# Performance work log

Measured on AMD Instinct MI355X. Metric: run time of the kernel, lower is better.

## Reference

```python
import jax, jax.numpy as jnp
import numpy as np

D_MODEL = 768
NHEAD = 12
HEAD_DIM = D_MODEL // NHEAD


def setup_inputs() -> dict:
    key = jax.random.key(0)
    ks = jax.random.split(key, 7)
    s = 1.0 / np.sqrt(D_MODEL)
    x = jax.random.normal(ks[0], (8, 1024, D_MODEL), dtype=jnp.float32)
    Wq = jax.random.uniform(ks[1], (D_MODEL, D_MODEL), jnp.float32, -s, s)
    bq = jax.random.uniform(ks[2], (D_MODEL,), jnp.float32, -s, s)
    Wk = jax.random.uniform(ks[3], (D_MODEL, D_MODEL), jnp.float32, -s, s)
    bk = jax.random.uniform(ks[4], (D_MODEL,), jnp.float32, -s, s)
    Wv = jax.random.uniform(ks[5], (D_MODEL, D_MODEL), jnp.float32, -s, s)
    bv = jax.random.uniform(ks[6], (D_MODEL,), jnp.float32, -s, s)
    return {"x": x, "Wq": Wq, "bq": bq, "Wk": Wk, "bk": bk, "Wv": Wv, "bv": bv}


def reference(x, Wq, bq, Wk, bk, Wv, bv):
    B, S, D = x.shape
    # linear projections (torch Linear: x @ W.T + b)
    q = x @ Wq.T + bq
    k = x @ Wk.T + bk
    v = x @ Wv.T + bv
    # split heads: [B, S, H, Dh] -> [B, H, S, Dh]
    split = lambda t: t.reshape(B, S, NHEAD, HEAD_DIM).transpose(0, 2, 1, 3)
    q, k, v = split(q), split(k), split(v)
    scale = 1.0 / np.sqrt(HEAD_DIM)
    scores = jnp.einsum("bhqd,bhkd->bhqk", q, k) * scale  # [B,H,S,S]
    scores = jax.nn.softmax(scores, axis=-1)  # dropout p=0.0 -> identity
    h = jnp.einsum("bhqk,bhkd->bhqd", scores, v)  # [B,H,S,Dh]
    h = h.transpose(0, 2, 1, 3).reshape(B, S, D)
    return (h, scores)
```

## Files before the change

kernel.cpp:

```cpp
#include <hip/hip_runtime.h>

#define D_MODEL  768
#define NHEAD    12
#define HEAD_DIM 64
#define SEQ      1024
#define BATCH    8
#define NTOK     8192

typedef unsigned short u16;
typedef unsigned int   u32;
typedef float  f32x4  __attribute__((ext_vector_type(4)));
typedef __bf16 bf16x8 __attribute__((ext_vector_type(8)));

#define MFMA(a, b, c) __builtin_amdgcn_mfma_f32_16x16x32_bf16((a), (b), (c), 0, 0, 0)

__device__ __forceinline__ u16 f2bf(float f) {
    u32 u = __float_as_uint(f);
    u += 0x7fffu + ((u >> 16) & 1u);
    return (u16)(u >> 16);
}
__device__ __forceinline__ u32 pack2(float a, float b) {
    return (u32)f2bf(a) | ((u32)f2bf(b) << 16);
}
__device__ __forceinline__ bf16x8 ldfrag(const u16* p) {
    union { uint4 u; bf16x8 b; } c;
    c.u = *(const uint4*)p;
    return c.b;
}

__global__ __launch_bounds__(256)
void qkv_gemm(const float* __restrict__ x,
              const float* __restrict__ Wq, const float* __restrict__ bq,
              const float* __restrict__ Wk, const float* __restrict__ bk,
              const float* __restrict__ Wv, const float* __restrict__ bv,
              u16* __restrict__ qo, u16* __restrict__ ko, u16* __restrict__ vto)
{
    const int m0 = blockIdx.x * 64;
    const int n0 = blockIdx.y * 64;
    const int z  = blockIdx.z;
    const float* W    = (z == 0) ? Wq : (z == 1) ? Wk : Wv;
    const float* bias = (z == 0) ? bq : (z == 1) ? bk : bv;

    __shared__ u16 As[64][72];
    __shared__ u16 Bs[64][72];

    const int t    = threadIdx.x;
    const int lane = t & 63, wave = t >> 6;
    const int grp  = lane >> 4, l16 = lane & 15;
    const int wm   = (wave >> 1) * 32;
    const int wn   = (wave & 1) * 32;
    const int sr   = t >> 2;
    const int sc   = (t & 3) * 16;

    f32x4 acc[2][2] = {};

    for (int kt = 0; kt < D_MODEL; kt += 64) {
        const float* xp = x + (size_t)(m0 + sr) * D_MODEL + kt + sc;
        const float* wp = W + (size_t)(n0 + sr) * D_MODEL + kt + sc;
        const float4 x0 = ((const float4*)xp)[0], x1 = ((const float4*)xp)[1];
        const float4 x2 = ((const float4*)xp)[2], x3 = ((const float4*)xp)[3];
        const float4 w0 = ((const float4*)wp)[0], w1 = ((const float4*)wp)[1];
        const float4 w2 = ((const float4*)wp)[2], w3 = ((const float4*)wp)[3];
        __syncthreads();
        uint4 ua, ub;
        ua.x = pack2(x0.x, x0.y); ua.y = pack2(x0.z, x0.w);
        ua.z = pack2(x1.x, x1.y); ua.w = pack2(x1.z, x1.w);
        ub.x = pack2(x2.x, x2.y); ub.y = pack2(x2.z, x2.w);
        ub.z = pack2(x3.x, x3.y); ub.w = pack2(x3.z, x3.w);
        *(uint4*)&As[sr][sc]     = ua;
        *(uint4*)&As[sr][sc + 8] = ub;
        ua.x = pack2(w0.x, w0.y); ua.y = pack2(w0.z, w0.w);
        ua.z = pack2(w1.x, w1.y); ua.w = pack2(w1.z, w1.w);
        ub.x = pack2(w2.x, w2.y); ub.y = pack2(w2.z, w2.w);
        ub.z = pack2(w3.x, w3.y); ub.w = pack2(w3.z, w3.w);
        *(uint4*)&Bs[sr][sc]     = ua;
        *(uint4*)&Bs[sr][sc + 8] = ub;
        __syncthreads();
#pragma unroll
        for (int ks = 0; ks < 64; ks += 32) {
            const bf16x8 a0 = ldfrag(&As[wm + l16][ks + grp * 8]);
            const bf16x8 a1 = ldfrag(&As[wm + 16 + l16][ks + grp * 8]);
            const bf16x8 b0 = ldfrag(&Bs[wn + l16][ks + grp * 8]);
            const bf16x8 b1 = ldfrag(&Bs[wn + 16 + l16][ks + grp * 8]);
            acc[0][0] = MFMA(a0, b0, acc[0][0]);
            acc[0][1] = MFMA(a0, b1, acc[0][1]);
            acc[1][0] = MFMA(a1, b0, acc[1][0]);
            acc[1][1] = MFMA(a1, b1, acc[1][1]);
        }
    }

    u16* qk_out = (z == 0) ? qo : ko;
#pragma unroll
    for (int tn = 0; tn < 2; ++tn) {
        const int col = n0 + wn + tn * 16 + l16;
        const float bcol = bias[col];
#pragma unroll
        for (int tm = 0; tm < 2; ++tm) {
#pragma unroll
            for (int r = 0; r < 4; ++r) {
                const int row = m0 + wm + tm * 16 + grp * 4 + r;
                const u16 hv = f2bf(acc[tm][tn][r] + bcol);
                if (z < 2) {
                    qk_out[(size_t)row * D_MODEL + col] = hv;
                } else {
                    const int hh = col >> 6, dd = col & 63;
                    const int bb = row >> 10, ss = row & 1023;
                    vto[(((size_t)(bb * NHEAD + hh)) * HEAD_DIM + dd) * SEQ + ss] = hv;
                }
            }
        }
    }
}

__global__ __launch_bounds__(256)
void attn_mfma(const u16* __restrict__ qb, const u16* __restrict__ kb,
               const u16* __restrict__ vtb, float* __restrict__ hout,
               float* __restrict__ sout)
{
    const int qt = blockIdx.x, h = blockIdx.y, b = blockIdx.z;
    const int t    = threadIdx.x;
    const int lane = t & 63, wave = t >> 6;
    const int grp  = lane >> 4, l16 = lane & 15;

    __shared__ u16 Qs[64][72];
    __shared__ u16 Ks[64][72];
    __shared__ u16 Vts[64][72];
    __shared__ u16 Ps[4][16][40];

    const size_t tok0 = (size_t)b * SEQ + qt * 64;
    const int    hb   = h * HEAD_DIM;
    const int    lr   = t >> 3, c0 = (t & 7) * 8;

    {
        const u16* qp = qb + (tok0 + lr) * D_MODEL + hb + c0;
        const uint4 v0 = *(const uint4*)qp;
        const uint4 v1 = *(const uint4*)(qp + (size_t)32 * D_MODEL);
        *(uint4*)&Qs[lr][c0]      = v0;
        *(uint4*)&Qs[lr + 32][c0] = v1;
    }
    __syncthreads();
    const bf16x8 qa0 = ldfrag(&Qs[wave * 16 + l16][grp * 8]);
    const bf16x8 qa1 = ldfrag(&Qs[wave * 16 + l16][32 + grp * 8]);

    const float scale = 0.125f;
    float ssum[4] = {0.f, 0.f, 0.f, 0.f};

    for (int kt = 0; kt < 16; ++kt) {
        __syncthreads();
        {
            const u16* kp = kb + ((size_t)b * SEQ + kt * 64 + lr) * D_MODEL + hb + c0;
            const uint4 v0 = *(const uint4*)kp;
            const uint4 v1 = *(const uint4*)(kp + (size_t)32 * D_MODEL);
            *(uint4*)&Ks[lr][c0]      = v0;
            *(uint4*)&Ks[lr + 32][c0] = v1;
        }
        __syncthreads();
#pragma unroll
        for (int ti = 0; ti < 4; ++ti) {
            const bf16x8 kb0 = ldfrag(&Ks[ti * 16 + l16][grp * 8]);
            const bf16x8 kb1 = ldfrag(&Ks[ti * 16 + l16][32 + grp * 8]);
            f32x4 c = {0.f, 0.f, 0.f, 0.f};
            c = MFMA(qa0, kb0, c);
            c = MFMA(qa1, kb1, c);
#pragma unroll
            for (int r = 0; r < 4; ++r) ssum[r] += __expf(c[r] * scale);
        }
    }
#pragma unroll
    for (int off = 1; off < 16; off <<= 1)
#pragma unroll
        for (int r = 0; r < 4; ++r) ssum[r] += __shfl_xor(ssum[r], off);
    float sinv[4];
#pragma unroll
    for (int r = 0; r < 4; ++r) sinv[r] = 1.0f / ssum[r];

    f32x4 accO[4] = {};
    float* sp = sout + (size_t)(b * NHEAD + h) * SEQ * SEQ;

    for (int kt = 0; kt < 16; ++kt) {
        __syncthreads();
        {
            const u16* kp = kb + ((size_t)b * SEQ + kt * 64 + lr) * D_MODEL + hb + c0;
            const uint4 v0 = *(const uint4*)kp;
            const uint4 v1 = *(const uint4*)(kp + (size_t)32 * D_MODEL);
            *(uint4*)&Ks[lr][c0]      = v0;
            *(uint4*)&Ks[lr + 32][c0] = v1;
            const u16* vp = vtb + ((size_t)(b * NHEAD + h) * HEAD_DIM + lr) * SEQ + kt * 64 + c0;
            const uint4 u0 = *(const uint4*)vp;
            const uint4 u1 = *(const uint4*)(vp + (size_t)32 * SEQ);
            *(uint4*)&Vts[lr][c0]      = u0;
            *(uint4*)&Vts[lr + 32][c0] = u1;
        }
        __syncthreads();
#pragma unroll
        for (int half = 0; half < 2; ++half) {
#pragma unroll
            for (int sub = 0; sub < 2; ++sub) {
                const int ti = half * 2 + sub;
                const bf16x8 kb0 = ldfrag(&Ks[ti * 16 + l16][grp * 8]);
                const bf16x8 kb1 = ldfrag(&Ks[ti * 16 + l16][32 + grp * 8]);
                f32x4 c = {0.f, 0.f, 0.f, 0.f};
                c = MFMA(qa0, kb0, c);
                c = MFMA(qa1, kb1, c);
#pragma unroll
                for (int r = 0; r < 4; ++r) {
                    const float p = __expf(c[r] * scale) * sinv[r];
                    const int qrow = qt * 64 + wave * 16 + grp * 4 + r;
                    sp[(size_t)qrow * SEQ + kt * 64 + ti * 16 + l16] = p;
                    Ps[wave][grp * 4 + r][sub * 16 + l16] = f2bf(p);
                }
            }
            const bf16x8 pa = ldfrag(&Ps[wave][l16][grp * 8]);
#pragma unroll
            for (int c4 = 0; c4 < 4; ++c4) {
                const bf16x8 vb = ldfrag(&Vts[c4 * 16 + l16][half * 32 + grp * 8]);
                accO[c4] = MFMA(pa, vb, accO[c4]);
            }
        }
    }

#pragma unroll
    for (int c4 = 0; c4 < 4; ++c4)
#pragma unroll
        for (int r = 0; r < 4; ++r)
            hout[(tok0 + wave * 16 + grp * 4 + r) * D_MODEL + hb + c4 * 16 + l16] =
                accO[c4][r];
}

extern "C" void kernel_launch(void* const* d_in, const int* in_sizes, int n_in,
                              void* d_out, int out_size, void* d_ws, size_t ws_size,
                              hipStream_t stream)
{
    const float* x  = (const float*)d_in[0];
    const float* Wq = (const float*)d_in[1];
    const float* bq = (const float*)d_in[2];
    const float* Wk = (const float*)d_in[3];
    const float* bk = (const float*)d_in[4];
    const float* Wv = (const float*)d_in[5];
    const float* bv = (const float*)d_in[6];

    float* hout = (float*)d_out;
    float* sout = hout + (size_t)NTOK * D_MODEL;

    u16* qbuf  = (u16*)d_ws;
    u16* kbuf  = qbuf + (size_t)NTOK * D_MODEL;
    u16* vtbuf = kbuf + (size_t)NTOK * D_MODEL;

    qkv_gemm<<<dim3(NTOK / 64, D_MODEL / 64, 3), 256, 0, stream>>>(
        x, Wq, bq, Wk, bk, Wv, bv, qbuf, kbuf, vtbuf);
    attn_mfma<<<dim3(SEQ / 64, NHEAD, BATCH), 256, 0, stream>>>(
        qbuf, kbuf, vtbuf, hout, sout);
}
```

Baseline: 646.7 us.

## Fuse softmax passes into one, deferring normalization and buffering probabilities in registers

Removes the separate first pass over K that only computed softmax row sums. Unnormalized exp values are now accumulated into row sums and fed to the PV MFMA in a single sweep, with the 1/sum normalization applied to the output at the end. The bf16 probability fragments are kept in 32 uint4 registers and written to the scores output afterwards as normalized float4 stores. This roughly halves the QK^T MFMA, exp and K-load work, and makes the score stores vectorized. In exchange, register pressure rises a lot under launch_bounds(256,2), so spills are possible, and the scores output is now rounded to bf16 precision instead of being exact fp32.

```diff
diff --git a/kernel.cpp b/kernel.cpp
--- a/kernel.cpp
+++ b/kernel.cpp
@@ -27,6 +27,13 @@
     c.u = *(const uint4*)p;
     return c.b;
 }
+__device__ __forceinline__ bf16x8 u2b(uint4 u) {
+    union { uint4 u; bf16x8 b; } c;
+    c.u = u;
+    return c.b;
+}
+__device__ __forceinline__ float bflo(u32 u) { return __uint_as_float(u << 16); }
+__device__ __forceinline__ float bfhi(u32 u) { return __uint_as_float(u & 0xffff0000u); }
 
 __global__ __launch_bounds__(256)
 void qkv_gemm(const float* __restrict__ x,
@@ -112,7 +119,7 @@
     }
 }
 
-__global__ __launch_bounds__(256)
+__global__ __launch_bounds__(256, 2)
 void attn_mfma(const u16* __restrict__ qb, const u16* __restrict__ kb,
                const u16* __restrict__ vtb, float* __restrict__ hout,
                float* __restrict__ sout)
@@ -144,50 +151,24 @@
 
     const float scale = 0.125f;
     float ssum[4] = {0.f, 0.f, 0.f, 0.f};
-
+    f32x4 accO[4] = {};
+    uint4 preg[32];
+
+    const u16* kbase = kb + (size_t)b * SEQ * D_MODEL + hb;
+    const u16* vbase = vtb + ((size_t)(b * NHEAD + h) * HEAD_DIM + lr) * SEQ;
+
+#pragma unroll
     for (int kt = 0; kt < 16; ++kt) {
         __syncthreads();
         {
-            const u16* kp = kb + ((size_t)b * SEQ + kt * 64 + lr) * D_MODEL + hb + c0;
+            const u16* kp = kbase + (size_t)(kt * 64 + lr) * D_MODEL + c0;
             const uint4 v0 = *(const uint4*)kp;
             const uint4 v1 = *(const uint4*)(kp + (size_t)32 * D_MODEL);
-            *(uint4*)&Ks[lr][c0]      = v0;
-            *(uint4*)&Ks[lr + 32][c0] = v1;
-        }
-        __syncthreads();
-#pragma unroll
-        for (int ti = 0; ti < 4; ++ti) {
-            const bf16x8 kb0 = ldfrag(&Ks[ti * 16 + l16][grp * 8]);
-            const bf16x8 kb1 = ldfrag(&Ks[ti * 16 + l16][32 + grp * 8]);
-            f32x4 c = {0.f, 0.f, 0.f, 0.f};
-            c = MFMA(qa0, kb0, c);
-            c = MFMA(qa1, kb1, c);
-#pragma unroll
-            for (int r = 0; r < 4; ++r) ssum[r] += __expf(c[r] * scale);
-        }
-    }
-#pragma unroll
-    for (int off = 1; off < 16; off <<= 1)
-#pragma unroll
-        for (int r = 0; r < 4; ++r) ssum[r] += __shfl_xor(ssum[r], off);
-    float sinv[4];
-#pragma unroll
-    for (int r = 0; r < 4; ++r) sinv[r] = 1.0f / ssum[r];
-
-    f32x4 accO[4] = {};
-    float* sp = sout + (size_t)(b * NHEAD + h) * SEQ * SEQ;
-
-    for (int kt = 0; kt < 16; ++kt) {
-        __syncthreads();
-        {
-            const u16* kp = kb + ((size_t)b * SEQ + kt * 64 + lr) * D_MODEL + hb + c0;
-            const uint4 v0 = *(const uint4*)kp;
-            const uint4 v1 = *(const uint4*)(kp + (size_t)32 * D_MODEL);
-            *(uint4*)&Ks[lr][c0]      = v0;
-            *(uint4*)&Ks[lr + 32][c0] = v1;
-            const u16* vp = vtb + ((size_t)(b * NHEAD + h) * HEAD_DIM + lr) * SEQ + kt * 64 + c0;
+            const u16* vp = vbase + kt * 64 + c0;
             const uint4 u0 = *(const uint4*)vp;
             const uint4 u1 = *(const uint4*)(vp + (size_t)32 * SEQ);
+            *(uint4*)&Ks[lr][c0]       = v0;
+            *(uint4*)&Ks[lr + 32][c0]  = v1;
             *(uint4*)&Vts[lr][c0]      = u0;
             *(uint4*)&Vts[lr + 32][c0] = u1;
         }
@@ -204,13 +185,14 @@
                 c = MFMA(qa1, kb1, c);
 #pragma unroll
                 for (int r = 0; r < 4; ++r) {
-                    const float p = __expf(c[r] * scale) * sinv[r];
-                    const int qrow = qt * 64 + wave * 16 + grp * 4 + r;
-                    sp[(size_t)qrow * SEQ + kt * 64 + ti * 16 + l16] = p;
+                    const float p = __expf(c[r] * scale);
+                    ssum[r] += p;
                     Ps[wave][grp * 4 + r][sub * 16 + l16] = f2bf(p);
                 }
             }
-            const bf16x8 pa = ldfrag(&Ps[wave][l16][grp * 8]);
+            const uint4 pw = *(const uint4*)&Ps[wave][l16][grp * 8];
+            preg[kt * 2 + half] = pw;
+            const bf16x8 pa = u2b(pw);
 #pragma unroll
             for (int c4 = 0; c4 < 4; ++c4) {
                 const bf16x8 vb = ldfrag(&Vts[c4 * 16 + l16][half * 32 + grp * 8]);
@@ -220,11 +202,43 @@
     }
 
 #pragma unroll
+    for (int off = 1; off < 16; off <<= 1)
+#pragma unroll
+        for (int r = 0; r < 4; ++r) ssum[r] += __shfl_xor(ssum[r], off);
+    float sinv[4];
+#pragma unroll
+    for (int r = 0; r < 4; ++r) sinv[r] = 1.0f / ssum[r];
+
+    const int src = (l16 >> 2) * 16 + l16;
+    const float t0 = __shfl(ssum[0], src), t1 = __shfl(ssum[1], src);
+    const float t2 = __shfl(ssum[2], src), t3 = __shfl(ssum[3], src);
+    const float sa = (l16 & 1) ? t1 : t0;
+    const float sb = (l16 & 1) ? t3 : t2;
+    const float sinvrow = 1.0f / ((l16 & 2) ? sb : sa);
+
+#pragma unroll
     for (int c4 = 0; c4 < 4; ++c4)
 #pragma unroll
         for (int r = 0; r < 4; ++r)
             hout[(tok0 + wave * 16 + grp * 4 + r) * D_MODEL + hb + c4 * 16 + l16] =
-                accO[c4][r];
+                accO[c4][r] * sinv[r];
+
+    float* sp = sout + (size_t)(b * NHEAD + h) * SEQ * SEQ
+              + (size_t)(qt * 64 + wave * 16 + l16) * SEQ + grp * 8;
+#pragma unroll
+    for (int kt = 0; kt < 16; ++kt) {
+#pragma unroll
+        for (int half = 0; half < 2; ++half) {
+            const uint4 pw = preg[kt * 2 + half];
+            float4 o0, o1;
+            o0.x = bflo(pw.x) * sinvrow; o0.y = bfhi(pw.x) * sinvrow;
+            o0.z = bflo(pw.y) * sinvrow; o0.w = bfhi(pw.y) * sinvrow;
+            o1.x = bflo(pw.z) * sinvrow; o1.y = bfhi(pw.z) * sinvrow;
+            o1.z = bflo(pw.w) * sinvrow; o1.w = bfhi(pw.w) * sinvrow;
+            *(float4*)(sp + kt * 64 + half * 32)     = o0;
+            *(float4*)(sp + kt * 64 + half * 32 + 4) = o1;
+        }
+    }
 }
 
 extern "C" void kernel_launch(void* const* d_in, const int* in_sizes, int n_in,
```

After: 630.3 us. -2.5%, faster.
